# Performance work log

Measured on AMD Instinct MI355X. Metric: run time of the kernel, lower is better.

Reference implementation:

```python
import jax, jax.numpy as jnp
import numpy as np

B, T, D, H, HD = 128, 256, 512, 8, 64

def setup_inputs() -> dict:
    key = jax.random.key(0)
    ks = jax.random.split(key, 5)
    scale = 0.02
    return {
        "x": jax.random.normal(ks[0], (B, T, D), dtype=jnp.float32),
        "Wq": jax.random.normal(ks[1], (H, D, HD), dtype=jnp.float32) * scale,
        "Wk": jax.random.normal(ks[2], (H, D, HD), dtype=jnp.float32) * scale,
        "Wv": jax.random.normal(ks[3], (H, D, HD), dtype=jnp.float32) * scale,
        "Wo": jax.random.normal(ks[4], (D, D), dtype=jnp.float32) * scale,
        "bo": jnp.zeros((D,), dtype=jnp.float32),
    }

def reference(x, Wq, Wk, Wv, Wo, bo):
    # Per-head projections, batched over heads: [B,T,D] x [H,D,HD] -> [B,H,T,HD]
    q = jnp.einsum('btd,hdk->bhtk', x, Wq)
    k = jnp.einsum('btd,hdk->bhtk', x, Wk)
    v = jnp.einsum('btd,hdk->bhtk', x, Wv)
    # Scaled scores [B,H,T,T] with causal mask
    scores = jnp.einsum('bhtk,bhsk->bhts', q, k) * (HD ** -0.5)
    causal = jnp.tril(jnp.ones((T, T), dtype=bool))
    scores = jnp.where(causal, scores, jnp.finfo(scores.dtype).min)
    attn = jax.nn.softmax(scores, axis=-1)
    # Dropout is identity at inference.
    out = jnp.einsum('bhts,bhsk->bhtk', attn, v)
    # Concat heads: [B,T,H*HD] == [B,T,D]
    out = out.transpose(0, 2, 1, 3).reshape(B, T, D)
    # Output projection
    return out @ Wo + bo
```

## Files before the change

kernel.cpp:

```cpp
#include <hip/hip_runtime.h>
#include <hip/hip_bf16.h>

typedef __bf16 bf16x8 __attribute__((ext_vector_type(8)));
typedef __bf16 bf16x4 __attribute__((ext_vector_type(4)));
typedef float f32x4 __attribute__((ext_vector_type(4)));
typedef unsigned short u16x8 __attribute__((ext_vector_type(8)));


__device__ __forceinline__ unsigned short f2bf(float f) {
  unsigned u = __float_as_uint(f);
  u += 0x7fffu + ((u >> 16) & 1u);
  return (unsigned short)(u >> 16);
}

__device__ __forceinline__ bf16x4 cvt4(f32x4 v) {
  bf16x4 o;
  o[0] = (__bf16)v[0]; o[1] = (__bf16)v[1]; o[2] = (__bf16)v[2]; o[3] = (__bf16)v[3];
  return o;
}

__device__ __forceinline__ void async16(const void* g, void* l) {
  __builtin_amdgcn_global_load_lds(
      (const __attribute__((address_space(1))) void*)g,
      (__attribute__((address_space(3))) void*)l, 16, 0, 0);
}

__global__ __launch_bounds__(256) void k_convert_x(const float* __restrict__ in,
                                                   unsigned short* __restrict__ out) {
  int i = blockIdx.x * 256 + threadIdx.x;
  const float4* p = (const float4*)in + (size_t)i * 2;
  float4 a = p[0], b = p[1];
  u16x8 o;
  o[0] = f2bf(a.x); o[1] = f2bf(a.y); o[2] = f2bf(a.z); o[3] = f2bf(a.w);
  o[4] = f2bf(b.x); o[5] = f2bf(b.y); o[6] = f2bf(b.z); o[7] = f2bf(b.w);
  *((u16x8*)out + i) = o;
}

__global__ __launch_bounds__(256) void k_transpose_w3(const float* __restrict__ w0,
                                                      const float* __restrict__ w1,
                                                      const float* __restrict__ w2,
                                                      unsigned short* __restrict__ out) {
  __shared__ unsigned short tile[64][72];
  int z = blockIdx.z;
  int wsel = z >> 3, hsel = z & 7;
  const float* inb = (wsel == 0 ? w0 : (wsel == 1 ? w1 : w2)) + (size_t)hsel * 512 * 64;
  unsigned short* outb = out + (size_t)z * 512 * 64;
  int r0 = blockIdx.y * 64;
  int tid = threadIdx.x;
  int r = tid >> 2, cq = (tid & 3) * 16;
  const float* src = inb + (size_t)(r0 + r) * 64 + cq;
#pragma unroll
  for (int i = 0; i < 16; i += 4) {
    float4 v = *(const float4*)(src + i);
    tile[r][cq + i + 0] = f2bf(v.x);
    tile[r][cq + i + 1] = f2bf(v.y);
    tile[r][cq + i + 2] = f2bf(v.z);
    tile[r][cq + i + 3] = f2bf(v.w);
  }
  __syncthreads();
  int cr = tid >> 2, rq = (tid & 3) * 16;
  u16x8 o0, o1;
#pragma unroll
  for (int i = 0; i < 8; ++i) o0[i] = tile[rq + i][cr];
#pragma unroll
  for (int i = 0; i < 8; ++i) o1[i] = tile[rq + 8 + i][cr];
  unsigned short* dst = outb + (size_t)cr * 512 + r0 + rq;
  *(u16x8*)dst = o0;
  *(u16x8*)(dst + 8) = o1;
}

__global__ __launch_bounds__(256) void k_transpose_w(const float* __restrict__ in,
                                                     unsigned short* __restrict__ out,
                                                     int rows, int cols) {
  __shared__ unsigned short tile[64][72];
  int c0 = blockIdx.x * 64, r0 = blockIdx.y * 64;
  int tid = threadIdx.x;
  int r = tid >> 2, cq = (tid & 3) * 16;
  const float* src = in + (size_t)(r0 + r) * cols + c0 + cq;
#pragma unroll
  for (int i = 0; i < 16; i += 4) {
    float4 v = *(const float4*)(src + i);
    tile[r][cq + i + 0] = f2bf(v.x);
    tile[r][cq + i + 1] = f2bf(v.y);
    tile[r][cq + i + 2] = f2bf(v.z);
    tile[r][cq + i + 3] = f2bf(v.w);
  }
  __syncthreads();
  int cr = tid >> 2, rq = (tid & 3) * 16;
  u16x8 o0, o1;
#pragma unroll
  for (int i = 0; i < 8; ++i) o0[i] = tile[rq + i][cr];
#pragma unroll
  for (int i = 0; i < 8; ++i) o1[i] = tile[rq + 8 + i][cr];
  unsigned short* dst = out + (size_t)(c0 + cr) * rows + r0 + rq;
  *(u16x8*)dst = o0;
  *(u16x8*)(dst + 8) = o1;
}

template <int KIND>
__global__ __launch_bounds__(512, 1) void k_gemmP(
    const unsigned short* __restrict__ A,
    const unsigned short* __restrict__ Bmat,
    unsigned short* __restrict__ O0,
    unsigned short* __restrict__ O1,
    const float* __restrict__ bo,
    float* __restrict__ outf) {
  __shared__ unsigned short smem[65536];
  const int P = (KIND == 0) ? 64 : 32;
  int xcd = blockIdx.x & 7, g = blockIdx.x >> 3;
  int w = xcd * P + g;
  int mt, nt;
  if (KIND == 0) { mt = w >> 2; nt = w & 3; }
  else           { mt = w >> 1; nt = w & 1; }
  int m0 = mt * 256, n0 = nt * 256;
  int tid = threadIdx.x;
  int wid = tid >> 6, lane = tid & 63;
  int lr = lane & 15, lg = lane >> 4;
  int wm = wid >> 2, wn = wid & 3;

  int srow = wid * 16 + (lane >> 3);
  int scs = (lane & 7) ^ (lane >> 3);
  auto stage_tile = [&](int kb, int buf) {
#pragma unroll
    for (int H = 0; H < 4; ++H) {
      const unsigned short* gb = (H < 2) ? (A + (size_t)(m0 + H * 128) * 512)
                                         : (Bmat + (size_t)(n0 + (H - 2) * 128) * 512);
#pragma unroll
      for (int j = 0; j < 2; ++j) {
        int row = srow + j * 8;
        async16(gb + (size_t)row * 512 + kb * 64 + scs * 8,
                smem + buf * 32768 + H * 8192 + (wid * 2 + j) * 512);
      }
    }
  };
  int xcol0 = ((0 * 64 + lg * 16) ^ ((lr & 7) * 16)) >> 1;
  int xcol1 = ((1 * 64 + lg * 16) ^ ((lr & 7) * 16)) >> 1;
  auto lda = [&](int buf, int mi, int k32) -> bf16x8 {
    int off = buf * 32768 + wm * 8192 + (mi * 16 + lr) * 64 + (k32 ? xcol1 : xcol0);
    return *(const bf16x8*)&smem[off];
  };
  auto ldb = [&](int buf, int ni, int k32) -> bf16x8 {
    int n = wn * 64 + ni * 16 + lr;
    int off = buf * 32768 + 16384 + (n >> 7) * 8192 + (n & 127) * 64 + (k32 ? xcol1 : xcol0);
    return *(const bf16x8*)&smem[off];
  };

  f32x4 acc[8][4];
#pragma unroll
  for (int mi = 0; mi < 8; ++mi)
#pragma unroll
    for (int ni = 0; ni < 4; ++ni) acc[mi][ni] = (f32x4){0.f, 0.f, 0.f, 0.f};

#define MF(dst, afrag, bfrag)                                                        \
  if constexpr (KIND == 2)                                                           \
    dst = __builtin_amdgcn_mfma_f32_16x16x32_bf16(afrag, bfrag, dst, 0, 0, 0);       \
  else                                                                               \
    dst = __builtin_amdgcn_mfma_f32_16x16x32_bf16(bfrag, afrag, dst, 0, 0, 0);

  stage_tile(0, 0);
  stage_tile(1, 1);
  asm volatile("s_waitcnt vmcnt(8)" ::: "memory");
  __builtin_amdgcn_s_barrier();
  asm volatile("" ::: "memory");

  bf16x8 a03[4][2], a47[4][2], b01[2][2], b23[2][2];
#pragma unroll
  for (int t = 0; t < 8; ++t) {
    int buf = t & 1;
#pragma unroll
    for (int mi = 0; mi < 4; ++mi) {
      a03[mi][0] = lda(buf, mi, 0);     a03[mi][1] = lda(buf, mi, 1);
      a47[mi][0] = lda(buf, mi + 4, 0); a47[mi][1] = lda(buf, mi + 4, 1);
    }
#pragma unroll
    for (int ni = 0; ni < 2; ++ni) {
      b01[ni][0] = ldb(buf, ni, 0);     b01[ni][1] = ldb(buf, ni, 1);
      b23[ni][0] = ldb(buf, ni + 2, 0); b23[ni][1] = ldb(buf, ni + 2, 1);
    }
    __builtin_amdgcn_s_setprio(1);
#pragma unroll
    for (int mi = 0; mi < 4; ++mi)
#pragma unroll
      for (int ni = 0; ni < 2; ++ni)
#pragma unroll
        for (int k = 0; k < 2; ++k) { MF(acc[mi][ni], a03[mi][k], b01[ni][k]); }
#pragma unroll
    for (int mi = 0; mi < 4; ++mi)
#pragma unroll
      for (int ni = 0; ni < 2; ++ni)
#pragma unroll
        for (int k = 0; k < 2; ++k) { MF(acc[mi + 4][ni], a47[mi][k], b01[ni][k]); }
    __builtin_amdgcn_s_setprio(0);
    asm volatile("s_waitcnt lgkmcnt(0)" ::: "memory");
    __builtin_amdgcn_s_barrier();
    asm volatile("" ::: "memory");
    if (t < 6) stage_tile(t + 2, buf);
    __builtin_amdgcn_s_setprio(1);
#pragma unroll
    for (int mi = 0; mi < 4; ++mi)
#pragma unroll
      for (int ni = 0; ni < 2; ++ni)
#pragma unroll
        for (int k = 0; k < 2; ++k) { MF(acc[mi][ni + 2], a03[mi][k], b23[ni][k]); }
#pragma unroll
    for (int mi = 0; mi < 4; ++mi)
#pragma unroll
      for (int ni = 0; ni < 2; ++ni)
#pragma unroll
        for (int k = 0; k < 2; ++k) { MF(acc[mi + 4][ni + 2], a47[mi][k], b23[ni][k]); }
    __builtin_amdgcn_s_setprio(0);
    if (t < 6)       asm volatile("s_waitcnt vmcnt(8)" ::: "memory");
    else if (t == 6) asm volatile("s_waitcnt vmcnt(0)" ::: "memory");
    asm volatile("" ::: "memory");
    __builtin_amdgcn_s_barrier();
    asm volatile("" ::: "memory");
  }
#undef MF

  if constexpr (KIND == 0) {
    int z = n0 >> 9;
    int h = ((n0 + wn * 64) >> 6) & 7;
    unsigned short* outp = (z ? O1 : O0) + (size_t)(mt * 8 + h) * 16384;
#pragma unroll
    for (int ni = 0; ni < 4; ++ni) {
      int hd0 = ni * 16 + lg * 4;
#pragma unroll
      for (int mi = 0; mi < 8; ++mi) {
        int tq = wm * 128 + mi * 16 + lr;
        *(bf16x4*)&outp[(size_t)tq * 64 + hd0] = cvt4(acc[mi][ni]);
      }
    }
  } else if constexpr (KIND == 1) {
#pragma unroll
    for (int ni = 0; ni < 4; ++ni) {
      int nb = n0 + wn * 64 + ni * 16 + lg * 4;
      float4 b4 = *(const float4*)&bo[nb];
#pragma unroll
      for (int mi = 0; mi < 8; ++mi) {
        int mg = m0 + wm * 128 + mi * 16 + lr;
        float4 o;
        o.x = acc[mi][ni][0] + b4.x; o.y = acc[mi][ni][1] + b4.y;
        o.z = acc[mi][ni][2] + b4.z; o.w = acc[mi][ni][3] + b4.w;
        *(float4*)&outf[(size_t)mg * 512 + nb] = o;
      }
    }
  } else {
    int h = (n0 >> 6) + wn;
    unsigned short* outp = O0 + (size_t)(mt * 8 + h) * 16384;
#pragma unroll
    for (int ni = 0; ni < 4; ++ni) {
      int hd = ni * 16 + lr;
#pragma unroll
      for (int mi = 0; mi < 8; ++mi) {
        int tq = wm * 128 + mi * 16 + lg * 4;
        *(bf16x4*)&outp[(size_t)hd * 256 + tq] = cvt4(acc[mi][ni]);
      }
    }
  }
}

__global__ __launch_bounds__(512, 1) void k_attn2(
    const unsigned short* __restrict__ Qb,
    const unsigned short* __restrict__ Kb,
    const unsigned short* __restrict__ Vtb,
    unsigned short* __restrict__ Ob) {
  __shared__ unsigned short Ks[16384];
  __shared__ unsigned short Vs[16384];
  __shared__ unsigned short Ps[8][16][264];
  int bh = blockIdx.x;
  int tid = threadIdx.x, wid = tid >> 6, lane = tid & 63, lr = lane & 15, lg = lane >> 4;
  int bb = bh >> 3, h = bh & 7;
  const unsigned short* Kg = Kb + (size_t)bh * 16384;
  const unsigned short* Vg = Vtb + (size_t)bh * 16384;
#pragma unroll
  for (int c = 0; c < 4; ++c) {
    int d = (wid * 4 + c) * 64 + lane;
    int kr = d >> 3, kc = (d & 7) ^ (kr & 7);
    async16(Kg + (size_t)kr * 64 + kc * 8, Ks + (wid * 4 + c) * 512);
    int vr = d >> 5, vc = (d & 31) ^ ((vr & 7) << 2);
    async16(Vg + (size_t)vr * 256 + vc * 8, Vs + (wid * 4 + c) * 512);
  }
  __syncthreads();

#pragma unroll
  for (int cc = 0; cc < 2; ++cc) {
    int ci = cc ? (15 - wid) : wid;
    int t0 = ci * 16, trow = t0 + lr;
    int ntV = ci + 1;
    int ntE = (ntV + 1) & ~1;
    int nk32 = ntE >> 1;
    const unsigned short* qsrc = Qb + (size_t)bh * 16384 + (size_t)(t0 + lr) * 64 + lg * 8;
    bf16x8 bq0 = *(const bf16x8*)qsrc;
    bf16x8 bq1 = *(const bf16x8*)(qsrc + 32);
    f32x4 acc[16];
#pragma unroll
    for (int nt = 0; nt < 16; ++nt)
      if (nt < ntE) acc[nt] = (f32x4){0.f, 0.f, 0.f, 0.f};
#pragma unroll
    for (int nt = 0; nt < 16; ++nt)
      if (nt < ntV) {
        int row = nt * 16 + lr;
        bf16x8 ak0 = *(const bf16x8*)&Ks[row * 64 + ((0 + lg) ^ (lr & 7)) * 8];
        acc[nt] = __builtin_amdgcn_mfma_f32_16x16x32_bf16(ak0, bq0, acc[nt], 0, 0, 0);
        bf16x8 ak1 = *(const bf16x8*)&Ks[row * 64 + ((4 + lg) ^ (lr & 7)) * 8];
        acc[nt] = __builtin_amdgcn_mfma_f32_16x16x32_bf16(ak1, bq1, acc[nt], 0, 0, 0);
      }
    float m = -3.0e38f;
#pragma unroll
    for (int nt = 0; nt < 16; ++nt)
      if (nt < ntE) {
#pragma unroll
        for (int r = 0; r < 4; ++r) {
          float v = acc[nt][r] * 0.125f;
          if (nt * 16 + lg * 4 + r > trow) v = -1.0e30f;
          acc[nt][r] = v;
          m = fmaxf(m, v);
        }
      }
    m = fmaxf(m, __shfl_xor(m, 16));
    m = fmaxf(m, __shfl_xor(m, 32));
    float s = 0.f;
#pragma unroll
    for (int nt = 0; nt < 16; ++nt)
      if (nt < ntE) {
        bf16x4 pk;
#pragma unroll
        for (int r = 0; r < 4; ++r) {
          float p = __expf(acc[nt][r] - m);
          s += p;
          pk[r] = (__bf16)p;
        }
        *(bf16x4*)&Ps[wid][lr][nt * 16 + lg * 4] = pk;
      }
    s += __shfl_xor(s, 16);
    s += __shfl_xor(s, 32);
    float inv = 1.0f / s;
    __threadfence_block();
    f32x4 aco[4];
#pragma unroll
    for (int vt = 0; vt < 4; ++vt) aco[vt] = (f32x4){0.f, 0.f, 0.f, 0.f};
#pragma unroll
    for (int k32 = 0; k32 < 8; ++k32)
      if (k32 < nk32) {
        bf16x8 pb = *(const bf16x8*)&Ps[wid][lr][k32 * 32 + lg * 8];
#pragma unroll
        for (int vt = 0; vt < 4; ++vt) {
          int row = vt * 16 + lr;
          bf16x8 av = *(const bf16x8*)&Vs[row * 256 + (((k32 * 4 + lg) ^ ((lr & 7) << 2)) * 8)];
          aco[vt] = __builtin_amdgcn_mfma_f32_16x16x32_bf16(av, pb, aco[vt], 0, 0, 0);
        }
      }
    unsigned short* obase = Ob + (size_t)(bb * 256 + trow) * 512 + h * 64 + lg * 4;
#pragma unroll
    for (int vt = 0; vt < 4; ++vt) {
      bf16x4 ov;
#pragma unroll
      for (int r = 0; r < 4; ++r) ov[r] = (__bf16)(aco[vt][r] * inv);
      *(bf16x4*)(obase + vt * 16) = ov;
    }
    __threadfence_block();
  }
}

extern "C" void kernel_launch(void* const* d_in, const int* in_sizes, int n_in,
                              void* d_out, int out_size, void* d_ws, size_t ws_size,
                              hipStream_t stream) {
  (void)in_sizes; (void)n_in; (void)out_size; (void)ws_size;
  const float* x = (const float*)d_in[0];
  const float* Wq = (const float*)d_in[1];
  const float* Wk = (const float*)d_in[2];
  const float* Wv = (const float*)d_in[3];
  const float* Wo = (const float*)d_in[4];
  const float* bo = (const float*)d_in[5];
  float* out = (float*)d_out;
  char* ws = (char*)d_ws;
  const size_t MB = 1024 * 1024;
  unsigned short* Qb = (unsigned short*)(ws);
  unsigned short* Kb = (unsigned short*)(ws + 32 * MB);
  unsigned short* Vtb = (unsigned short*)(ws + 64 * MB);
  unsigned short* xb = (unsigned short*)(ws + 96 * MB);
  unsigned short* Wqt = (unsigned short*)(ws + 128 * MB);
  unsigned short* Wkt = Wqt + 262144;
  unsigned short* Wvt = Wkt + 262144;
  unsigned short* Wot = Wvt + 262144;

  hipLaunchKernelGGL(k_convert_x, dim3(8192), dim3(256), 0, stream, x, xb);
  hipLaunchKernelGGL(k_transpose_w3, dim3(1, 8, 24), dim3(256), 0, stream, Wq, Wk, Wv, Wqt);
  hipLaunchKernelGGL(k_transpose_w, dim3(8, 8, 1), dim3(256), 0, stream, Wo, Wot, 512, 512);
  hipLaunchKernelGGL((k_gemmP<0>), dim3(512), dim3(512), 0, stream,
                     xb, Wqt, Qb, Kb, (const float*)nullptr, (float*)nullptr);
  hipLaunchKernelGGL((k_gemmP<2>), dim3(256), dim3(512), 0, stream,
                     xb, Wvt, Vtb, (unsigned short*)nullptr, (const float*)nullptr, (float*)nullptr);
  hipLaunchKernelGGL(k_attn2, dim3(1024), dim3(512), 0, stream, Qb, Kb, Vtb, xb);
  hipLaunchKernelGGL((k_gemmP<1>), dim3(256), dim3(512), 0, stream,
                     xb, Wot, (unsigned short*)nullptr, (unsigned short*)nullptr, bo, out);
}
```

Measured before the change: 184.0 us.

## Split GEMM K-loop into four quarter-tile stages with interleaved async loads

Rewrites the GEMM main loop so each k-step prefetches the next tile in four quarter pieces (A half 0, B half 0, A half 1, B half 1), each issued between MFMA quarters with barriers and vmcnt waits, replacing the two-deep whole-tile prefetch. The warp-to-tile mapping changes to interleaved rows and columns (mi*32+wm*16, ni*64+wn*16), and the epilogue indexing is updated to match. The aim is to spread global-to-LDS traffic across the compute phases and reduce stalls. In exchange it adds more barriers per step and effectively uses only one tile of prefetch lookahead.

```diff
diff --git a/kernel.cpp b/kernel.cpp
--- a/kernel.cpp
+++ b/kernel.cpp
@@ -118,31 +118,33 @@
   int lr = lane & 15, lg = lane >> 4;
   int wm = wid >> 2, wn = wid & 3;
 
-  int srow = wid * 16 + (lane >> 3);
-  int scs = (lane & 7) ^ (lane >> 3);
-  auto stage_tile = [&](int kb, int buf) {
-#pragma unroll
-    for (int H = 0; H < 4; ++H) {
-      const unsigned short* gb = (H < 2) ? (A + (size_t)(m0 + H * 128) * 512)
-                                         : (Bmat + (size_t)(n0 + (H - 2) * 128) * 512);
-#pragma unroll
-      for (int j = 0; j < 2; ++j) {
-        int row = srow + j * 8;
-        async16(gb + (size_t)row * 512 + kb * 64 + scs * 8,
-                smem + buf * 32768 + H * 8192 + (wid * 2 + j) * 512);
-      }
+  int srow_off = wid * 16 + (lane >> 3);
+  int schunk = (lane & 7) ^ (lane >> 3);
+  auto stageA = [&](int kb, int buf, int half) {
+#pragma unroll
+    for (int j = 0; j < 2; ++j) {
+      int row = half * 128 + srow_off + j * 8;
+      async16(A + (size_t)(m0 + row) * 512 + kb * 64 + schunk * 8,
+              smem + buf * 32768 + half * 8192 + (wid * 2 + j) * 512);
     }
   };
-  int xcol0 = ((0 * 64 + lg * 16) ^ ((lr & 7) * 16)) >> 1;
-  int xcol1 = ((1 * 64 + lg * 16) ^ ((lr & 7) * 16)) >> 1;
+  auto stageB = [&](int kb, int buf, int half) {
+#pragma unroll
+    for (int j = 0; j < 2; ++j) {
+      int row = half * 128 + srow_off + j * 8;
+      async16(Bmat + (size_t)(n0 + row) * 512 + kb * 64 + schunk * 8,
+              smem + buf * 32768 + 16384 + half * 8192 + (wid * 2 + j) * 512);
+    }
+  };
   auto lda = [&](int buf, int mi, int k32) -> bf16x8 {
-    int off = buf * 32768 + wm * 8192 + (mi * 16 + lr) * 64 + (k32 ? xcol1 : xcol0);
-    return *(const bf16x8*)&smem[off];
+    int row = mi * 32 + wm * 16 + lr;
+    int ch = (k32 * 4 + lg) ^ (lr & 7);
+    return *(const bf16x8*)&smem[buf * 32768 + row * 64 + ch * 8];
   };
   auto ldb = [&](int buf, int ni, int k32) -> bf16x8 {
-    int n = wn * 64 + ni * 16 + lr;
-    int off = buf * 32768 + 16384 + (n >> 7) * 8192 + (n & 127) * 64 + (k32 ? xcol1 : xcol0);
-    return *(const bf16x8*)&smem[off];
+    int row = ni * 64 + wn * 16 + lr;
+    int ch = (k32 * 4 + lg) ^ (lr & 7);
+    return *(const bf16x8*)&smem[buf * 32768 + 16384 + row * 64 + ch * 8];
   };
 
   f32x4 acc[8][4];
@@ -156,27 +158,26 @@
     dst = __builtin_amdgcn_mfma_f32_16x16x32_bf16(afrag, bfrag, dst, 0, 0, 0);       \
   else                                                                               \
     dst = __builtin_amdgcn_mfma_f32_16x16x32_bf16(bfrag, afrag, dst, 0, 0, 0);
-
-  stage_tile(0, 0);
-  stage_tile(1, 1);
-  asm volatile("s_waitcnt vmcnt(8)" ::: "memory");
+#define BAR_LGKM()                                      \
+  __builtin_amdgcn_s_barrier();                         \
+  asm volatile("s_waitcnt lgkmcnt(0)" ::: "memory");
+
+  stageA(0, 0, 0); stageB(0, 0, 0); stageA(0, 0, 1); stageB(0, 0, 1);
+  asm volatile("s_waitcnt vmcnt(4)" ::: "memory");
   __builtin_amdgcn_s_barrier();
   asm volatile("" ::: "memory");
 
   bf16x8 a03[4][2], a47[4][2], b01[2][2], b23[2][2];
 #pragma unroll
   for (int t = 0; t < 8; ++t) {
-    int buf = t & 1;
-#pragma unroll
-    for (int mi = 0; mi < 4; ++mi) {
-      a03[mi][0] = lda(buf, mi, 0);     a03[mi][1] = lda(buf, mi, 1);
-      a47[mi][0] = lda(buf, mi + 4, 0); a47[mi][1] = lda(buf, mi + 4, 1);
-    }
-#pragma unroll
-    for (int ni = 0; ni < 2; ++ni) {
-      b01[ni][0] = ldb(buf, ni, 0);     b01[ni][1] = ldb(buf, ni, 1);
-      b23[ni][0] = ldb(buf, ni + 2, 0); b23[ni][1] = ldb(buf, ni + 2, 1);
-    }
+    int buf = t & 1, nbuf = buf ^ 1;
+    const bool st = (t < 7);
+#pragma unroll
+    for (int mi = 0; mi < 4; ++mi) { a03[mi][0] = lda(buf, mi, 0); a03[mi][1] = lda(buf, mi, 1); }
+#pragma unroll
+    for (int ni = 0; ni < 2; ++ni) { b01[ni][0] = ldb(buf, ni, 0); b01[ni][1] = ldb(buf, ni, 1); }
+    if (st) stageA(t + 1, nbuf, 0);
+    BAR_LGKM();
     __builtin_amdgcn_s_setprio(1);
 #pragma unroll
     for (int mi = 0; mi < 4; ++mi)
@@ -184,6 +185,16 @@
       for (int ni = 0; ni < 2; ++ni)
 #pragma unroll
         for (int k = 0; k < 2; ++k) { MF(acc[mi][ni], a03[mi][k], b01[ni][k]); }
+    __builtin_amdgcn_s_setprio(0);
+    if (st) asm volatile("s_waitcnt vmcnt(4)" ::: "memory");
+    else    asm volatile("s_waitcnt vmcnt(2)" ::: "memory");
+    __builtin_amdgcn_s_barrier();
+    asm volatile("" ::: "memory");
+#pragma unroll
+    for (int mi = 0; mi < 4; ++mi) { a47[mi][0] = lda(buf, mi + 4, 0); a47[mi][1] = lda(buf, mi + 4, 1); }
+    if (st) stageB(t + 1, nbuf, 0);
+    BAR_LGKM();
+    __builtin_amdgcn_s_setprio(1);
 #pragma unroll
     for (int mi = 0; mi < 4; ++mi)
 #pragma unroll
@@ -191,17 +202,15 @@
 #pragma unroll
         for (int k = 0; k < 2; ++k) { MF(acc[mi + 4][ni], a47[mi][k], b01[ni][k]); }
     __builtin_amdgcn_s_setprio(0);
-    asm volatile("s_waitcnt lgkmcnt(0)" ::: "memory");
+    if (st) asm volatile("s_waitcnt vmcnt(4)" ::: "memory");
+    else    asm volatile("s_waitcnt vmcnt(0)" ::: "memory");
     __builtin_amdgcn_s_barrier();
     asm volatile("" ::: "memory");
-    if (t < 6) stage_tile(t + 2, buf);
+#pragma unroll
+    for (int ni = 0; ni < 2; ++ni) { b23[ni][0] = ldb(buf, ni + 2, 0); b23[ni][1] = ldb(buf, ni + 2, 1); }
+    if (st) stageA(t + 1, nbuf, 1);
+    BAR_LGKM();
     __builtin_amdgcn_s_setprio(1);
-#pragma unroll
-    for (int mi = 0; mi < 4; ++mi)
-#pragma unroll
-      for (int ni = 0; ni < 2; ++ni)
-#pragma unroll
-        for (int k = 0; k < 2; ++k) { MF(acc[mi][ni + 2], a03[mi][k], b23[ni][k]); }
 #pragma unroll
     for (int mi = 0; mi < 4; ++mi)
 #pragma unroll
@@ -209,35 +218,47 @@
 #pragma unroll
         for (int k = 0; k < 2; ++k) { MF(acc[mi + 4][ni + 2], a47[mi][k], b23[ni][k]); }
     __builtin_amdgcn_s_setprio(0);
-    if (t < 6)       asm volatile("s_waitcnt vmcnt(8)" ::: "memory");
-    else if (t == 6) asm volatile("s_waitcnt vmcnt(0)" ::: "memory");
-    asm volatile("" ::: "memory");
+    if (st) asm volatile("s_waitcnt vmcnt(4)" ::: "memory");
     __builtin_amdgcn_s_barrier();
     asm volatile("" ::: "memory");
+    if (st) stageB(t + 1, nbuf, 1);
+    __builtin_amdgcn_s_barrier();
+    __builtin_amdgcn_s_setprio(1);
+#pragma unroll
+    for (int mi = 0; mi < 4; ++mi)
+#pragma unroll
+      for (int ni = 0; ni < 2; ++ni)
+#pragma unroll
+        for (int k = 0; k < 2; ++k) { MF(acc[mi][ni + 2], a03[mi][k], b23[ni][k]); }
+    __builtin_amdgcn_s_setprio(0);
+    if (st) asm volatile("s_waitcnt vmcnt(4)" ::: "memory");
+    __builtin_amdgcn_s_barrier();
+    asm volatile("" ::: "memory");
   }
 #undef MF
+#undef BAR_LGKM
 
   if constexpr (KIND == 0) {
     int z = n0 >> 9;
-    int h = ((n0 + wn * 64) >> 6) & 7;
-    unsigned short* outp = (z ? O1 : O0) + (size_t)(mt * 8 + h) * 16384;
+    int hbase = (n0 & 511) >> 6;
+    int hd0 = wn * 16 + lg * 4;
 #pragma unroll
     for (int ni = 0; ni < 4; ++ni) {
-      int hd0 = ni * 16 + lg * 4;
+      unsigned short* outp = (z ? O1 : O0) + (size_t)(mt * 8 + hbase + ni) * 16384;
 #pragma unroll
       for (int mi = 0; mi < 8; ++mi) {
-        int tq = wm * 128 + mi * 16 + lr;
+        int tq = mi * 32 + wm * 16 + lr;
         *(bf16x4*)&outp[(size_t)tq * 64 + hd0] = cvt4(acc[mi][ni]);
       }
     }
   } else if constexpr (KIND == 1) {
 #pragma unroll
     for (int ni = 0; ni < 4; ++ni) {
-      int nb = n0 + wn * 64 + ni * 16 + lg * 4;
+      int nb = n0 + ni * 64 + wn * 16 + lg * 4;
       float4 b4 = *(const float4*)&bo[nb];
 #pragma unroll
       for (int mi = 0; mi < 8; ++mi) {
-        int mg = m0 + wm * 128 + mi * 16 + lr;
+        int mg = m0 + mi * 32 + wm * 16 + lr;
         float4 o;
         o.x = acc[mi][ni][0] + b4.x; o.y = acc[mi][ni][1] + b4.y;
         o.z = acc[mi][ni][2] + b4.z; o.w = acc[mi][ni][3] + b4.w;
@@ -245,14 +266,14 @@
       }
     }
   } else {
-    int h = (n0 >> 6) + wn;
-    unsigned short* outp = O0 + (size_t)(mt * 8 + h) * 16384;
+    int hbase = n0 >> 6;
+    int hd = wn * 16 + lr;
 #pragma unroll
     for (int ni = 0; ni < 4; ++ni) {
-      int hd = ni * 16 + lr;
+      unsigned short* outp = O0 + (size_t)(mt * 8 + hbase + ni) * 16384;
 #pragma unroll
       for (int mi = 0; mi < 8; ++mi) {
-        int tq = wm * 128 + mi * 16 + lg * 4;
+        int tq = mi * 32 + wm * 16 + lg * 4;
         *(bf16x4*)&outp[(size_t)hd * 256 + tq] = cvt4(acc[mi][ni]);
       }
     }
```

After: 169.9 us. -7.6%, faster.
